# Kernel tuning notes

Hardware: AMD Instinct MI355X
Metric: run time of the kernel (lower is better)

## Reference

```python
import jax, jax.numpy as jnp
import numpy as np

T = 60          # fixed number of video frames (self.T)
EPS = 1e-5      # BatchNorm eps


def _lstm_cell(h, c, gates):
    # PyTorch gate order: input, forget, cell(g), output
    i, f, g, o = jnp.split(gates, 4, axis=-1)
    i = jax.nn.sigmoid(i)
    f = jax.nn.sigmoid(f)
    g = jnp.tanh(g)
    o = jax.nn.sigmoid(o)
    c = f * c + i * g
    h = o * jnp.tanh(c)
    return h, c


def setup_inputs() -> dict:
    key = jax.random.key(0)
    ks = jax.random.split(key, 12)
    B, H, Din, D = 256, 512, 2048, 512
    video_seq = jax.random.normal(ks[0], (B, T, Din), dtype=jnp.float32)
    captions = jax.random.randint(ks[1], (B, 20), 0, 10000, dtype=jnp.int32)
    s = 0.02
    return {
        'video_seq': video_seq,
        'captions': captions,
        'W_enc': jax.random.normal(ks[2], (D, Din), dtype=jnp.float32) * s,
        'b_enc': jnp.zeros((D,), jnp.float32),
        'gamma': jnp.ones((D,), jnp.float32),
        'beta': jnp.zeros((D,), jnp.float32),
        'w_attn': jax.random.normal(ks[3], (2 * H + T,), dtype=jnp.float32) * s,
        'b_attn': jnp.zeros((), jnp.float32),
        'W_ih': jax.random.normal(ks[4], (4 * H, D), dtype=jnp.float32) * s,
        'W_hh': jax.random.normal(ks[5], (4 * H, H), dtype=jnp.float32) * s,
        'b_ih': jnp.zeros((4 * H,), jnp.float32),
        'b_hh': jnp.zeros((4 * H,), jnp.float32),
    }


def reference(video_seq, captions, W_enc, b_enc, gamma, beta,
              w_attn, b_attn, W_ih, W_hh, b_ih, b_hh):
    H = W_hh.shape[1]
    B = video_seq.shape[0]
    caplen = captions.shape[1]

    # Dropout: eval mode (identity). Linear 2048 -> 512.
    v = jnp.einsum('btf,df->btd', video_seq, W_enc) + b_enc   # [B,T,512]
    # BatchNorm1d over channel dim (batch statistics, training-mode math)
    mean = v.mean(axis=(0, 1))
    var = v.var(axis=(0, 1))
    v = (v - mean) / jnp.sqrt(var + EPS) * gamma + beta       # [B,T,512]

    # Attention linear: concat([h,s,video_row]) @ w + b decomposes into
    # three independent dot products since h,s are broadcast over positions.
    w_h, w_s, w_v = w_attn[:H], w_attn[H:2 * H], w_attn[2 * H:]
    vscore = jnp.einsum('btd,t->bd', v, w_v) + b_attn         # [B,512]
    b_lstm = b_ih + b_hh

    v_t = jnp.moveaxis(v, 1, 0)                               # [T,B,512]

    def enc_step(carry, vt):
        h, c = carry
        scores = vscore + (h @ w_h + c @ w_s)[:, None]        # [B,512]
        alpha = jax.nn.softmax(scores, axis=1)
        x_t = alpha * vt                                      # [B,512]
        gates = x_t @ W_ih.T + h @ W_hh.T + b_lstm
        h, c = _lstm_cell(h, c, gates)
        return (h, c), h

    init = (jnp.zeros((B, H), v.dtype), jnp.zeros((B, H), v.dtype))
    (h, c), hs1 = jax.lax.scan(enc_step, init, v_t)           # hs1: [T,B,H]

    def pad_step(carry, _):
        h, c = carry
        gates = h @ W_hh.T + b_lstm                           # zero input
        h, c = _lstm_cell(h, c, gates)
        return (h, c), h

    _, hs2 = jax.lax.scan(pad_step, (h, c), None, length=caplen)
    hs = jnp.concatenate([hs1, hs2], axis=0)                  # [T+caplen,B,H]
    return jnp.transpose(hs, (1, 0, 2))                       # [B,T+caplen,H]
```

## Files before the change

### kernel.cpp

```cpp
#include <hip/hip_runtime.h>
#include <hip/hip_bf16.h>
#include <math.h>

#define B_    256
#define T_    60
#define TTOT  80
#define DIN   2048
#define D_    512
#define H_    512
#define G4    2048
#define M1    15360

typedef __bf16 bf16x8 __attribute__((ext_vector_type(8)));
typedef __bf16 bf16x4 __attribute__((ext_vector_type(4)));
typedef float  f32x4  __attribute__((ext_vector_type(4)));

__global__ void k_zero_u32(unsigned* __restrict__ p, int n) {
  int i = blockIdx.x * 256 + threadIdx.x;
  if (i < n) p[i] = 0u;
}

__global__ __launch_bounds__(256) void k_cvt(const float* __restrict__ s,
                                             __bf16* __restrict__ d, int n) {
  int i = (blockIdx.x * 256 + threadIdx.x) * 4;
  if (i >= n) return;
  float4 f = *(const float4*)(s + i);
  bf16x4 v;
  v[0] = (__bf16)f.x; v[1] = (__bf16)f.y; v[2] = (__bf16)f.z; v[3] = (__bf16)f.w;
  *(bf16x4*)(d + i) = v;
}

__global__ void k_bsum(const float* __restrict__ a, const float* __restrict__ b,
                       float* __restrict__ d) {
  int i = blockIdx.x * 256 + threadIdx.x;
  if (i < G4) d[i] = a[i] + b[i];
}

template<bool ALPHA, bool OUTBF, bool XT>
__global__ __launch_bounds__(256) void k_mm(const float* __restrict__ A, int lda,
                                            const __bf16* __restrict__ Bm,
                                            const float* __restrict__ bias0,
                                            const float* __restrict__ bias1,
                                            const float* __restrict__ alpha,
                                            void* __restrict__ Cout,
                                            int N, int K) {
  __shared__ __bf16 As[128 * 64];
  __shared__ __bf16 Bs[128 * 64];
  const int tid  = threadIdx.x;
  const int lane = tid & 63;
  const int wv   = tid >> 6;
  const int wm   = wv >> 1, wn = wv & 1;
  const int la   = lane & 15, lk = lane >> 4;

  int lin = blockIdx.y * gridDim.x + blockIdx.x;
  const int nwg = gridDim.x * gridDim.y;
  if ((nwg & 7) == 0) {
    int q = nwg >> 3;
    lin = (lin & 7) * q + (lin >> 3);
  }
  const int n0 = (lin % gridDim.x) * 128;
  const int m0 = (lin / gridDim.x) * 128;

  f32x4 acc[4][4];
  #pragma unroll
  for (int i = 0; i < 4; i++)
    #pragma unroll
    for (int j = 0; j < 4; j++) acc[i][j] = (f32x4){0.f, 0.f, 0.f, 0.f};

  for (int kt = 0; kt < K; kt += 64) {
    __syncthreads();
    #pragma unroll
    for (int i = 0; i < 4; i++) {
      int idx = tid + i * 256;
      int row = idx >> 3, gk = idx & 7;
      const float* src = A + (size_t)(m0 + row) * lda + kt + gk * 8;
      float4 f0 = *(const float4*)src;
      float4 f1 = *(const float4*)(src + 4);
      if (ALPHA) {
        int b = (m0 + row) / T_;
        const float* ap = alpha + (size_t)b * K + kt + gk * 8;
        float4 a0 = *(const float4*)ap;
        float4 a1 = *(const float4*)(ap + 4);
        f0.x *= a0.x; f0.y *= a0.y; f0.z *= a0.z; f0.w *= a0.w;
        f1.x *= a1.x; f1.y *= a1.y; f1.z *= a1.z; f1.w *= a1.w;
      }
      bf16x8 v;
      v[0] = (__bf16)f0.x; v[1] = (__bf16)f0.y; v[2] = (__bf16)f0.z; v[3] = (__bf16)f0.w;
      v[4] = (__bf16)f1.x; v[5] = (__bf16)f1.y; v[6] = (__bf16)f1.z; v[7] = (__bf16)f1.w;
      *(bf16x8*)(As + row * 64 + ((gk ^ (row & 7)) << 3)) = v;
    }
    #pragma unroll
    for (int i = 0; i < 4; i++) {
      int idx = tid + i * 256;
      int row = idx >> 3, gk = idx & 7;
      bf16x8 v = *(const bf16x8*)(Bm + (size_t)(n0 + row) * K + kt + gk * 8);
      *(bf16x8*)(Bs + row * 64 + ((gk ^ (row & 7)) << 3)) = v;
    }
    __syncthreads();
    #pragma unroll
    for (int ks = 0; ks < 2; ks++) {
      bf16x8 af[4], bfr[4];
      #pragma unroll
      for (int i = 0; i < 4; i++) {
        int row = wm * 64 + i * 16 + la;
        af[i] = *(const bf16x8*)(As + row * 64 + (((ks * 4 + lk) ^ (row & 7)) << 3));
      }
      #pragma unroll
      for (int j = 0; j < 4; j++) {
        int row = wn * 64 + j * 16 + la;
        bfr[j] = *(const bf16x8*)(Bs + row * 64 + (((ks * 4 + lk) ^ (row & 7)) << 3));
      }
      #pragma unroll
      for (int i = 0; i < 4; i++)
        #pragma unroll
        for (int j = 0; j < 4; j++)
          acc[i][j] = __builtin_amdgcn_mfma_f32_16x16x32_bf16(af[i], bfr[j], acc[i][j], 0, 0, 0);
    }
  }
  #pragma unroll
  for (int j = 0; j < 4; j++) {
    int col = n0 + wn * 64 + j * 16 + la;
    float bb = bias0[col] + (bias1 ? bias1[col] : 0.f);
    #pragma unroll
    for (int i = 0; i < 4; i++) {
      int rbase = m0 + wm * 64 + i * 16 + lk * 4;
      #pragma unroll
      for (int r = 0; r < 4; r++) {
        float v = acc[i][j][r] + bb;
        int m = rbase + r;
        if (XT) {
          int b = m / T_, tt = m % T_;
          int g = col >> 9, jj = col & 511;
          ((__bf16*)Cout)[(((size_t)tt * B_ + b) * 512 + jj) * 4 + g] = (__bf16)v;
        } else if (OUTBF) {
          ((__bf16*)Cout)[(size_t)m * N + col] = (__bf16)v;
        } else {
          ((float*)Cout)[(size_t)m * N + col] = v;
        }
      }
    }
  }
}

__global__ __launch_bounds__(256) void k_stats_partial(const float* __restrict__ V,
                                                       float* __restrict__ part) {
  const int blk = blockIdx.x;
  const int tid = threadIdx.x;
  float s0 = 0.f, s1 = 0.f, q0 = 0.f, q1 = 0.f;
  const float* p = V + (size_t)blk * 64 * D_;
  for (int r = 0; r < 64; r++) {
    float a = p[(size_t)r * D_ + tid];
    float b = p[(size_t)r * D_ + tid + 256];
    s0 += a; q0 += a * a;
    s1 += b; q1 += b * b;
  }
  part[(size_t)blk * 1024 + tid]             = s0;
  part[(size_t)blk * 1024 + tid + 256]       = s1;
  part[(size_t)blk * 1024 + 512 + tid]       = q0;
  part[(size_t)blk * 1024 + 512 + tid + 256] = q1;
}

__global__ __launch_bounds__(512) void k_stats_final(const float* __restrict__ part,
                                                     float* __restrict__ stats) {
  const int d = threadIdx.x;
  float s = 0.f, q = 0.f;
  for (int r = 0; r < 240; r++) {
    s += part[(size_t)r * 1024 + d];
    q += part[(size_t)r * 1024 + 512 + d];
  }
  float mean = s * (1.f / 15360.f);
  float var  = q * (1.f / 15360.f) - mean * mean;
  stats[d]        = mean;
  stats[512 + d]  = 1.f / sqrtf(var + 1e-5f);
}

__global__ __launch_bounds__(512) void k_norm_vscore(float* __restrict__ V,
                                                     const float* __restrict__ stats,
                                                     const float* __restrict__ gamma,
                                                     const float* __restrict__ beta,
                                                     const float* __restrict__ w_attn,
                                                     float* __restrict__ vscore) {
  const int b = blockIdx.x, d = threadIdx.x;
  __shared__ float wv[T_];
  if (d < T_) wv[d] = w_attn[2 * H_ + d];
  __syncthreads();
  const float mean = stats[d], rstd = stats[512 + d];
  const float ga = gamma[d], be = beta[d];
  float vs = 0.f;
  float* p = V + (size_t)b * T_ * D_ + d;
  for (int t = 0; t < T_; t++) {
    float x = p[(size_t)t * D_];
    float xn = (x - mean) * rstd * ga + be;
    p[(size_t)t * D_] = xn;
    vs += wv[t] * xn;
  }
  vscore[(size_t)b * D_ + d] = vs;
}

__global__ __launch_bounds__(512) void k_softmax(float* __restrict__ a) {
  const int b = blockIdx.x, d = threadIdx.x;
  __shared__ float red[8];
  float x = a[(size_t)b * D_ + d];
  float m = x;
  #pragma unroll
  for (int o = 32; o >= 1; o >>= 1) m = fmaxf(m, __shfl_xor(m, o));
  if ((d & 63) == 0) red[d >> 6] = m;
  __syncthreads();
  float M = red[0];
  #pragma unroll
  for (int w = 1; w < 8; w++) M = fmaxf(M, red[w]);
  float e = expf(x - M);
  float s = e;
  #pragma unroll
  for (int o = 32; o >= 1; o >>= 1) s += __shfl_xor(s, o);
  __syncthreads();
  if ((d & 63) == 0) red[d >> 6] = s;
  __syncthreads();
  float S = 0.f;
  #pragma unroll
  for (int w = 0; w < 8; w++) S += red[w];
  a[(size_t)b * D_ + d] = e / S;
}

__device__ __forceinline__ float sigf(float x) { return 1.f / (1.f + expf(-x)); }

__global__ __launch_bounds__(256) void k_rec(const __bf16* __restrict__ Whh,
                                             const __bf16* __restrict__ xW4,
                                             const float* __restrict__ bsum,
                                             __bf16* __restrict__ hbuf,
                                             float* __restrict__ out,
                                             unsigned* __restrict__ bar) {
  const int tid  = threadIdx.x;
  const int lane = tid & 63;
  const int widx = tid >> 6;
  const int grp  = blockIdx.x & 7;
  const int wg   = blockIdx.x >> 3;
  const int B0   = grp * 32;
  const int j0   = wg * 16;
  const int la   = lane & 15, lk = lane >> 4;

  __shared__ __bf16 wslab[4 * 16 * 520];
  __shared__ __bf16 hsin[16 * 520];
  __shared__ float  gatesL[4 * 256];

  #pragma unroll
  for (int it = 0; it < 16; it++) {
    bf16x8 v = *(const bf16x8*)(Whh + ((size_t)(widx * 512 + j0 + it)) * 512 + lane * 8);
    *(bf16x8*)(wslab + (widx * 16 + it) * 520 + lane * 8) = v;
  }

  const int cb = tid >> 4;
  const int cj = tid & 15;
  float bsl[4];
  #pragma unroll
  for (int g = 0; g < 4; g++) bsl[g] = bsum[g * 512 + j0 + cj];

  float creg[2] = {0.f, 0.f};
  unsigned* slots = bar + (size_t)grp * 64 * 32;

  bf16x4 xv[2];
  #pragma unroll
  for (int s = 0; s < 2; s++)
    xv[s] = *(const bf16x4*)(xW4 + (((size_t)(B0 + s * 16 + cb)) * 512 + j0 + cj) * 4);

  for (int t = 0; t < TTOT; t++) {
    const __bf16* hin  = hbuf + (size_t)(t & 1) * (B_ * H_);
    __bf16*       hout = hbuf + (size_t)((t + 1) & 1) * (B_ * H_);

    #pragma unroll
    for (int s = 0; s < 2; s++) {
      const int s16 = s * 16;

      if (t > 0) {
        if (tid < 32) {
          while (__hip_atomic_load(slots + (tid * 2 + s) * 32, __ATOMIC_RELAXED,
                                   __HIP_MEMORY_SCOPE_AGENT) < (unsigned)t)
            __builtin_amdgcn_s_sleep(1);
        }
        __syncthreads();

        unsigned long long vbuf[8];
        #pragma unroll
        for (int it = 0; it < 8; it++) {
          int idx = tid + it * 256;
          int row = idx >> 7, col4 = (idx & 127) * 4;
          vbuf[it] = __hip_atomic_load(
              (const unsigned long long*)(hin + (size_t)(B0 + s16 + row) * H_ + col4),
              __ATOMIC_RELAXED, __HIP_MEMORY_SCOPE_AGENT);
        }
        #pragma unroll
        for (int it = 0; it < 8; it++) {
          int idx = tid + it * 256;
          int row = idx >> 7, col4 = (idx & 127) * 4;
          *(unsigned long long*)(hsin + row * 520 + col4) = vbuf[it];
        }
        __syncthreads();

        f32x4 acc = (f32x4){0.f, 0.f, 0.f, 0.f};
        #pragma unroll
        for (int ks = 0; ks < 16; ks++) {
          bf16x8 w = *(const bf16x8*)(wslab + (widx * 16 + la) * 520 + ks * 32 + lk * 8);
          bf16x8 a = *(const bf16x8*)(hsin + la * 520 + ks * 32 + lk * 8);
          acc = __builtin_amdgcn_mfma_f32_16x16x32_bf16(a, w, acc, 0, 0, 0);
        }
        #pragma unroll
        for (int r = 0; r < 4; r++)
          gatesL[widx * 256 + (lk * 4 + r) * 16 + la] = acc[r];
        __syncthreads();
      }

      float p[4];
      #pragma unroll
      for (int g = 0; g < 4; g++)
        p[g] = (t > 0 ? gatesL[g * 256 + tid] : 0.f) + (float)xv[s][g];
      float gi = sigf(p[0]), gf = sigf(p[1]), gg = tanhf(p[2]), go = sigf(p[3]);
      float cn = gf * creg[s] + gi * gg;
      creg[s] = cn;
      float hn = go * tanhf(cn);

      __bf16 hb = (__bf16)hn;
      __hip_atomic_store((unsigned short*)(hout + (size_t)(B0 + s16 + cb) * H_ + j0 + cj),
                         *(unsigned short*)&hb,
                         __ATOMIC_RELAXED, __HIP_MEMORY_SCOPE_AGENT);
      asm volatile("s_waitcnt vmcnt(0)" ::: "memory");
      __syncthreads();
      if (tid == 0)
        __hip_atomic_store(slots + (wg * 2 + s) * 32, (unsigned)(t + 1),
                           __ATOMIC_RELAXED, __HIP_MEMORY_SCOPE_AGENT);

      out[((size_t)(B0 + s16 + cb) * TTOT + t) * D_ + j0 + cj] = hn;
      if (t + 1 < T_) {
        xv[s] = *(const bf16x4*)(xW4 + (((size_t)(t + 1) * B_ + B0 + s16 + cb) * 512 + j0 + cj) * 4);
      } else {
        #pragma unroll
        for (int g = 0; g < 4; g++) xv[s][g] = (__bf16)bsl[g];
      }
    }
  }
}

extern "C" void kernel_launch(void* const* d_in, const int* in_sizes, int n_in,
                              void* d_out, int out_size, void* d_ws, size_t ws_size,
                              hipStream_t stream) {
  const float* video  = (const float*)d_in[0];
  const float* W_enc  = (const float*)d_in[2];
  const float* b_enc  = (const float*)d_in[3];
  const float* gamma  = (const float*)d_in[4];
  const float* beta   = (const float*)d_in[5];
  const float* w_attn = (const float*)d_in[6];
  const float* W_ih   = (const float*)d_in[8];
  const float* W_hh   = (const float*)d_in[9];
  const float* b_ih   = (const float*)d_in[10];
  const float* b_hh   = (const float*)d_in[11];
  float* out = (float*)d_out;

  float*    base  = (float*)d_ws;
  float*    V     = base;                    size_t off = (size_t)M1 * D_;
  float*    part  = base + off;              off += 240 * 1024;
  float*    stats = base + off;              off += 1024;
  float*    alpha = base + off;              off += (size_t)B_ * D_;
  float*    bsum  = base + off;              off += G4;
  __bf16*   hbuf  = (__bf16*)(base + off);   off += (size_t)2 * B_ * H_ / 2;
  unsigned* bar   = (unsigned*)(base + off); off += 16384;
  __bf16*   xWbf  = (__bf16*)(base + off);   off += (size_t)M1 * G4 / 2;
  __bf16*   Wencb = (__bf16*)(base + off);   off += (size_t)D_ * DIN / 2;
  __bf16*   Wihb  = (__bf16*)(base + off);   off += (size_t)G4 * H_ / 2;
  __bf16*   Whhb  = (__bf16*)(base + off);   off += (size_t)G4 * H_ / 2;

  k_cvt<<<1024, 256, 0, stream>>>(W_enc, Wencb, D_ * DIN);
  k_cvt<<<1024, 256, 0, stream>>>(W_ih, Wihb, G4 * H_);
  k_cvt<<<1024, 256, 0, stream>>>(W_hh, Whhb, G4 * H_);
  k_bsum<<<8, 256, 0, stream>>>(b_ih, b_hh, bsum);

  k_zero_u32<<<64, 256, 0, stream>>>(bar, 16384);

  k_mm<false, false, false><<<dim3(4, 120), 256, 0, stream>>>(
      video, DIN, Wencb, b_enc, nullptr, nullptr, V, D_, DIN);

  k_stats_partial<<<240, 256, 0, stream>>>(V, part);
  k_stats_final<<<1, 512, 0, stream>>>(part, stats);
  k_norm_vscore<<<B_, 512, 0, stream>>>(V, stats, gamma, beta, w_attn, alpha);
  k_softmax<<<B_, 512, 0, stream>>>(alpha);

  k_mm<true, true, true><<<dim3(16, 120), 256, 0, stream>>>(
      V, D_, Wihb, b_ih, b_hh, alpha, (void*)xWbf, G4, D_);

  k_rec<<<256, 256, 0, stream>>>(Whhb, xWbf, bsum, hbuf, out, bar);
}
```

Baseline: 548.8 us.

## Collapse recurrent LSTM block to single wavefront with register-held h fragments

The persistent recurrent kernel now runs one 64-thread wavefront per block instead of four. That single wave computes all four gate tiles with MFMA, and it loads the h operand directly from global memory into registers rather than staging it through shared memory. This removes several block-wide barriers and an LDS round trip on the serial critical path, and output h is written as 8-byte chunks through a small staging tile. It also adds a bounded spin loop on the inter-block flags. The trade-off is four times more MFMA work per wave and per-lane global loads of h that are less well coalesced.

New measurement: 705.4 us. 1.29x slower.

```diff
diff --git a/kernel.cpp b/kernel.cpp
--- a/kernel.cpp
+++ b/kernel.cpp
@@ -224,44 +224,42 @@
 
 __device__ __forceinline__ float sigf(float x) { return 1.f / (1.f + expf(-x)); }
 
-__global__ __launch_bounds__(256) void k_rec(const __bf16* __restrict__ Whh,
-                                             const __bf16* __restrict__ xW4,
-                                             const float* __restrict__ bsum,
-                                             __bf16* __restrict__ hbuf,
-                                             float* __restrict__ out,
-                                             unsigned* __restrict__ bar) {
+__global__ __launch_bounds__(64) void k_rec(const __bf16* __restrict__ Whh,
+                                            const __bf16* __restrict__ xW4,
+                                            const float* __restrict__ bsum,
+                                            __bf16* __restrict__ hbuf,
+                                            float* __restrict__ out,
+                                            unsigned* __restrict__ bar) {
   const int tid  = threadIdx.x;
-  const int lane = tid & 63;
-  const int widx = tid >> 6;
   const int grp  = blockIdx.x & 7;
   const int wg   = blockIdx.x >> 3;
   const int B0   = grp * 32;
   const int j0   = wg * 16;
-  const int la   = lane & 15, lk = lane >> 4;
-
-  __shared__ __bf16 wslab[4 * 16 * 520];
-  __shared__ __bf16 hsin[16 * 520];
-  __shared__ float  gatesL[4 * 256];
-
-  #pragma unroll
-  for (int it = 0; it < 16; it++) {
-    bf16x8 v = *(const bf16x8*)(Whh + ((size_t)(widx * 512 + j0 + it)) * 512 + lane * 8);
-    *(bf16x8*)(wslab + (widx * 16 + it) * 520 + lane * 8) = v;
-  }
-
-  const int cb = tid >> 4;
-  const int cj = tid & 15;
+  const int la   = tid & 15, lk = tid >> 4;
+
+  __shared__ __bf16 wslab[4 * 16 * 528];
+  __shared__ __bf16 hstage[16][16];
+
+  for (int r = 0; r < 64; r++) {
+    int g = r >> 4, jr = r & 15;
+    bf16x8 v = *(const bf16x8*)(Whh + ((size_t)(g * 512 + j0 + jr)) * 512 + tid * 8);
+    *(bf16x8*)(wslab + r * 528 + tid * 8) = v;
+  }
+  __syncthreads();
+
   float bsl[4];
   #pragma unroll
-  for (int g = 0; g < 4; g++) bsl[g] = bsum[g * 512 + j0 + cj];
-
-  float creg[2] = {0.f, 0.f};
+  for (int g = 0; g < 4; g++) bsl[g] = bsum[g * 512 + j0 + la];
+
+  float creg[2][4] = {{0.f,0.f,0.f,0.f},{0.f,0.f,0.f,0.f}};
   unsigned* slots = bar + (size_t)grp * 64 * 32;
 
-  bf16x4 xv[2];
+  bf16x4 xv[2][4];
   #pragma unroll
   for (int s = 0; s < 2; s++)
-    xv[s] = *(const bf16x4*)(xW4 + (((size_t)(B0 + s * 16 + cb)) * 512 + j0 + cj) * 4);
+    #pragma unroll
+    for (int r = 0; r < 4; r++)
+      xv[s][r] = *(const bf16x4*)(xW4 + (((size_t)(B0 + s * 16 + lk * 4 + r)) * 512 + j0 + la) * 4);
 
   for (int t = 0; t < TTOT; t++) {
     const __bf16* hin  = hbuf + (size_t)(t & 1) * (B_ * H_);
@@ -271,70 +269,84 @@
     for (int s = 0; s < 2; s++) {
       const int s16 = s * 16;
 
+      f32x4 acc[4];
+      #pragma unroll
+      for (int g = 0; g < 4; g++) acc[g] = (f32x4){0.f, 0.f, 0.f, 0.f};
+
       if (t > 0) {
         if (tid < 32) {
-          while (__hip_atomic_load(slots + (tid * 2 + s) * 32, __ATOMIC_RELAXED,
-                                   __HIP_MEMORY_SCOPE_AGENT) < (unsigned)t)
+          for (int it = 0; it < (1 << 22); it++) {
+            if (__hip_atomic_load(slots + (tid * 2 + s) * 32, __ATOMIC_RELAXED,
+                                  __HIP_MEMORY_SCOPE_AGENT) >= (unsigned)t)
+              break;
             __builtin_amdgcn_s_sleep(1);
+          }
         }
-        __syncthreads();
-
-        unsigned long long vbuf[8];
-        #pragma unroll
-        for (int it = 0; it < 8; it++) {
-          int idx = tid + it * 256;
-          int row = idx >> 7, col4 = (idx & 127) * 4;
-          vbuf[it] = __hip_atomic_load(
-              (const unsigned long long*)(hin + (size_t)(B0 + s16 + row) * H_ + col4),
-              __ATOMIC_RELAXED, __HIP_MEMORY_SCOPE_AGENT);
-        }
-        #pragma unroll
-        for (int it = 0; it < 8; it++) {
-          int idx = tid + it * 256;
-          int row = idx >> 7, col4 = (idx & 127) * 4;
-          *(unsigned long long*)(hsin + row * 520 + col4) = vbuf[it];
-        }
-        __syncthreads();
-
-        f32x4 acc = (f32x4){0.f, 0.f, 0.f, 0.f};
+
+        union { unsigned long long u[2]; bf16x8 v; } afr[16];
+        const unsigned long long* hrow =
+            (const unsigned long long*)(hin + (size_t)(B0 + s16 + la) * H_);
         #pragma unroll
         for (int ks = 0; ks < 16; ks++) {
-          bf16x8 w = *(const bf16x8*)(wslab + (widx * 16 + la) * 520 + ks * 32 + lk * 8);
-          bf16x8 a = *(const bf16x8*)(hsin + la * 520 + ks * 32 + lk * 8);
-          acc = __builtin_amdgcn_mfma_f32_16x16x32_bf16(a, w, acc, 0, 0, 0);
+          afr[ks].u[0] = __hip_atomic_load(hrow + ks * 8 + lk * 2, __ATOMIC_RELAXED,
+                                           __HIP_MEMORY_SCOPE_AGENT);
+          afr[ks].u[1] = __hip_atomic_load(hrow + ks * 8 + lk * 2 + 1, __ATOMIC_RELAXED,
+                                           __HIP_MEMORY_SCOPE_AGENT);
         }
+
         #pragma unroll
-        for (int r = 0; r < 4; r++)
-          gatesL[widx * 256 + (lk * 4 + r) * 16 + la] = acc[r];
-        __syncthreads();
-      }
-
-      float p[4];
-      #pragma unroll
-      for (int g = 0; g < 4; g++)
-        p[g] = (t > 0 ? gatesL[g * 256 + tid] : 0.f) + (float)xv[s][g];
-      float gi = sigf(p[0]), gf = sigf(p[1]), gg = tanhf(p[2]), go = sigf(p[3]);
-      float cn = gf * creg[s] + gi * gg;
-      creg[s] = cn;
-      float hn = go * tanhf(cn);
-
-      __bf16 hb = (__bf16)hn;
-      __hip_atomic_store((unsigned short*)(hout + (size_t)(B0 + s16 + cb) * H_ + j0 + cj),
-                         *(unsigned short*)&hb,
-                         __ATOMIC_RELAXED, __HIP_MEMORY_SCOPE_AGENT);
+        for (int ks = 0; ks < 16; ks++) {
+          #pragma unroll
+          for (int g = 0; g < 4; g++) {
+            bf16x8 w = *(const bf16x8*)(wslab + (g * 16 + la) * 528 + ks * 32 + lk * 8);
+            acc[g] = __builtin_amdgcn_mfma_f32_16x16x32_bf16(afr[ks].v, w, acc[g], 0, 0, 0);
+          }
+        }
+      }
+
+      float hnv[4];
+      #pragma unroll
+      for (int r = 0; r < 4; r++) {
+        float gi = sigf(acc[0][r] + (float)xv[s][r][0]);
+        float gf = sigf(acc[1][r] + (float)xv[s][r][1]);
+        float gg = tanhf(acc[2][r] + (float)xv[s][r][2]);
+        float go = sigf(acc[3][r] + (float)xv[s][r][3]);
+        float cn = gf * creg[s][r] + gi * gg;
+        creg[s][r] = cn;
+        float hn = go * tanhf(cn);
+        hnv[r] = hn;
+        hstage[lk * 4 + r][la] = (__bf16)hn;
+      }
+      __syncthreads();
+
+      {
+        int row = tid >> 2, ch = tid & 3;
+        __hip_atomic_store(
+            (unsigned long long*)(hout + (size_t)(B0 + s16 + row) * H_ + j0 + ch * 4),
+            *(const unsigned long long*)&hstage[row][ch * 4],
+            __ATOMIC_RELAXED, __HIP_MEMORY_SCOPE_AGENT);
+      }
       asm volatile("s_waitcnt vmcnt(0)" ::: "memory");
-      __syncthreads();
       if (tid == 0)
         __hip_atomic_store(slots + (wg * 2 + s) * 32, (unsigned)(t + 1),
                            __ATOMIC_RELAXED, __HIP_MEMORY_SCOPE_AGENT);
 
-      out[((size_t)(B0 + s16 + cb) * TTOT + t) * D_ + j0 + cj] = hn;
+      #pragma unroll
+      for (int r = 0; r < 4; r++)
+        out[((size_t)(B0 + s16 + lk * 4 + r) * TTOT + t) * D_ + j0 + la] = hnv[r];
+
       if (t + 1 < T_) {
-        xv[s] = *(const bf16x4*)(xW4 + (((size_t)(t + 1) * B_ + B0 + s16 + cb) * 512 + j0 + cj) * 4);
+        #pragma unroll
+        for (int r = 0; r < 4; r++)
+          xv[s][r] = *(const bf16x4*)(xW4 +
+              (((size_t)(t + 1) * B_ + B0 + s16 + lk * 4 + r) * 512 + j0 + la) * 4);
       } else {
         #pragma unroll
-        for (int g = 0; g < 4; g++) xv[s][g] = (__bf16)bsl[g];
-      }
+        for (int r = 0; r < 4; r++)
+          #pragma unroll
+          for (int g = 0; g < 4; g++) xv[s][r][g] = (__bf16)bsl[g];
+      }
+      __syncthreads();
     }
   }
 }
@@ -385,5 +397,5 @@
   k_mm<true, true, true><<<dim3(16, 120), 256, 0, stream>>>(
       V, D_, Wihb, b_ih, b_hh, alpha, (void*)xWbf, G4, D_);
 
-  k_rec<<<256, 256, 0, stream>>>(Whhb, xWbf, bsum, hbuf, out, bar);
-}
+  k_rec<<<256, 64, 0, stream>>>(Whhb, xWbf, bsum, hbuf, out, bar);
+}
```

## Merge per-half recurrent sync into one step barrier and fuse prep kernels

Applied to the files above, without the earlier changes.

The recurrent kernel now waits once per timestep on both batch halves and computes both 16-row MFMA tiles together. It loads h directly from global into registers instead of staging it through shared memory, and publishes both halves' flags after a single barrier. This halves the number of cross-block synchronisations and LDS round-trips per step. The spin-wait now has a bounded iteration count. Separately, the weight conversions, bias sum and flag zeroing are fused into one launch, and softmax is fused into the normalisation kernel, cutting launch count.

Result: slower. 906.0 us (+65.1%).

```diff
diff --git a/kernel.cpp b/kernel.cpp
--- a/kernel.cpp
+++ b/kernel.cpp
@@ -15,25 +15,34 @@
 typedef __bf16 bf16x4 __attribute__((ext_vector_type(4)));
 typedef float  f32x4  __attribute__((ext_vector_type(4)));
 
-__global__ void k_zero_u32(unsigned* __restrict__ p, int n) {
-  int i = blockIdx.x * 256 + threadIdx.x;
-  if (i < n) p[i] = 0u;
-}
-
-__global__ __launch_bounds__(256) void k_cvt(const float* __restrict__ s,
-                                             __bf16* __restrict__ d, int n) {
-  int i = (blockIdx.x * 256 + threadIdx.x) * 4;
-  if (i >= n) return;
-  float4 f = *(const float4*)(s + i);
-  bf16x4 v;
-  v[0] = (__bf16)f.x; v[1] = (__bf16)f.y; v[2] = (__bf16)f.z; v[3] = (__bf16)f.w;
-  *(bf16x4*)(d + i) = v;
-}
-
-__global__ void k_bsum(const float* __restrict__ a, const float* __restrict__ b,
-                       float* __restrict__ d) {
-  int i = blockIdx.x * 256 + threadIdx.x;
-  if (i < G4) d[i] = a[i] + b[i];
+__global__ __launch_bounds__(256) void k_prep(const float* __restrict__ We,
+                                              const float* __restrict__ Wi,
+                                              const float* __restrict__ Wh,
+                                              __bf16* __restrict__ Web,
+                                              __bf16* __restrict__ Wib,
+                                              __bf16* __restrict__ Whb,
+                                              const float* __restrict__ bi,
+                                              const float* __restrict__ bh,
+                                              float* __restrict__ bsum,
+                                              unsigned* __restrict__ flags) {
+  const int blk = blockIdx.x, tid = threadIdx.x;
+  if (blk < 3072) {
+    const float* s; __bf16* d; int base;
+    if (blk < 1024)      { s = We; d = Web; base = blk; }
+    else if (blk < 2048) { s = Wi; d = Wib; base = blk - 1024; }
+    else                 { s = Wh; d = Whb; base = blk - 2048; }
+    int i = (base * 256 + tid) * 4;
+    float4 f = *(const float4*)(s + i);
+    bf16x4 v;
+    v[0] = (__bf16)f.x; v[1] = (__bf16)f.y; v[2] = (__bf16)f.z; v[3] = (__bf16)f.w;
+    *(bf16x4*)(d + i) = v;
+  } else if (blk < 3080) {
+    int i = (blk - 3072) * 256 + tid;
+    bsum[i] = bi[i] + bh[i];
+  } else {
+    int i = (blk - 3080) * 256 + tid;
+    flags[i] = 0u;
+  }
 }
 
 template<bool ALPHA, bool OUTBF, bool XT>
@@ -174,14 +183,15 @@
   stats[512 + d]  = 1.f / sqrtf(var + 1e-5f);
 }
 
-__global__ __launch_bounds__(512) void k_norm_vscore(float* __restrict__ V,
-                                                     const float* __restrict__ stats,
-                                                     const float* __restrict__ gamma,
-                                                     const float* __restrict__ beta,
-                                                     const float* __restrict__ w_attn,
-                                                     float* __restrict__ vscore) {
+__global__ __launch_bounds__(512) void k_norm_alpha(float* __restrict__ V,
+                                                    const float* __restrict__ stats,
+                                                    const float* __restrict__ gamma,
+                                                    const float* __restrict__ beta,
+                                                    const float* __restrict__ w_attn,
+                                                    float* __restrict__ alpha) {
   const int b = blockIdx.x, d = threadIdx.x;
   __shared__ float wv[T_];
+  __shared__ float red[8];
   if (d < T_) wv[d] = w_attn[2 * H_ + d];
   __syncthreads();
   const float mean = stats[d], rstd = stats[512 + d];
@@ -194,14 +204,7 @@
     p[(size_t)t * D_] = xn;
     vs += wv[t] * xn;
   }
-  vscore[(size_t)b * D_ + d] = vs;
-}
-
-__global__ __launch_bounds__(512) void k_softmax(float* __restrict__ a) {
-  const int b = blockIdx.x, d = threadIdx.x;
-  __shared__ float red[8];
-  float x = a[(size_t)b * D_ + d];
-  float m = x;
+  float m = vs;
   #pragma unroll
   for (int o = 32; o >= 1; o >>= 1) m = fmaxf(m, __shfl_xor(m, o));
   if ((d & 63) == 0) red[d >> 6] = m;
@@ -209,7 +212,7 @@
   float M = red[0];
   #pragma unroll
   for (int w = 1; w < 8; w++) M = fmaxf(M, red[w]);
-  float e = expf(x - M);
+  float e = expf(vs - M);
   float s = e;
   #pragma unroll
   for (int o = 32; o >= 1; o >>= 1) s += __shfl_xor(s, o);
@@ -219,17 +222,17 @@
   float S = 0.f;
   #pragma unroll
   for (int w = 0; w < 8; w++) S += red[w];
-  a[(size_t)b * D_ + d] = e / S;
+  alpha[(size_t)b * D_ + d] = e / S;
 }
 
 __device__ __forceinline__ float sigf(float x) { return 1.f / (1.f + expf(-x)); }
 
-__global__ __launch_bounds__(256) void k_rec(const __bf16* __restrict__ Whh,
-                                             const __bf16* __restrict__ xW4,
-                                             const float* __restrict__ bsum,
-                                             __bf16* __restrict__ hbuf,
-                                             float* __restrict__ out,
-                                             unsigned* __restrict__ bar) {
+__global__ __launch_bounds__(256, 1) void k_rec(const __bf16* __restrict__ Whh,
+                                                const __bf16* __restrict__ xW4,
+                                                const float* __restrict__ bsum,
+                                                __bf16* __restrict__ hbuf,
+                                                float* __restrict__ out,
+                                                unsigned* __restrict__ bar) {
   const int tid  = threadIdx.x;
   const int lane = tid & 63;
   const int widx = tid >> 6;
@@ -240,8 +243,7 @@
   const int la   = lane & 15, lk = lane >> 4;
 
   __shared__ __bf16 wslab[4 * 16 * 520];
-  __shared__ __bf16 hsin[16 * 520];
-  __shared__ float  gatesL[4 * 256];
+  __shared__ float  gatesL[2][1024];
 
   #pragma unroll
   for (int it = 0; it < 16; it++) {
@@ -263,78 +265,100 @@
   for (int s = 0; s < 2; s++)
     xv[s] = *(const bf16x4*)(xW4 + (((size_t)(B0 + s * 16 + cb)) * 512 + j0 + cj) * 4);
 
+  __syncthreads();
+
   for (int t = 0; t < TTOT; t++) {
     const __bf16* hin  = hbuf + (size_t)(t & 1) * (B_ * H_);
     __bf16*       hout = hbuf + (size_t)((t + 1) & 1) * (B_ * H_);
 
+    if (t > 0) {
+      if (tid < 64) {
+        unsigned* p = slots + ((tid & 31) * 2 + (tid >> 5)) * 32;
+        for (int it = 0; it < (1 << 22); it++) {
+          if (__hip_atomic_load(p, __ATOMIC_RELAXED,
+                                __HIP_MEMORY_SCOPE_AGENT) >= (unsigned)t)
+            break;
+          __builtin_amdgcn_s_sleep(1);
+        }
+      }
+      __syncthreads();
+
+      const unsigned long long* r0 =
+          (const unsigned long long*)(hin + (size_t)(B0 + la) * H_);
+      const unsigned long long* r1 =
+          (const unsigned long long*)(hin + (size_t)(B0 + 16 + la) * H_);
+      unsigned long long a0[32], a1[32];
+      #pragma unroll
+      for (int ks = 0; ks < 16; ks++) {
+        a0[2 * ks]     = __hip_atomic_load(r0 + ks * 8 + lk * 2, __ATOMIC_RELAXED,
+                                           __HIP_MEMORY_SCOPE_AGENT);
+        a0[2 * ks + 1] = __hip_atomic_load(r0 + ks * 8 + lk * 2 + 1, __ATOMIC_RELAXED,
+                                           __HIP_MEMORY_SCOPE_AGENT);
+      }
+      #pragma unroll
+      for (int ks = 0; ks < 16; ks++) {
+        a1[2 * ks]     = __hip_atomic_load(r1 + ks * 8 + lk * 2, __ATOMIC_RELAXED,
+                                           __HIP_MEMORY_SCOPE_AGENT);
+        a1[2 * ks + 1] = __hip_atomic_load(r1 + ks * 8 + lk * 2 + 1, __ATOMIC_RELAXED,
+                                           __HIP_MEMORY_SCOPE_AGENT);
+      }
+
+      f32x4 acc0 = (f32x4){0.f, 0.f, 0.f, 0.f};
+      f32x4 acc1 = (f32x4){0.f, 0.f, 0.f, 0.f};
+      #pragma unroll
+      for (int ks = 0; ks < 16; ks++) {
+        bf16x8 w = *(const bf16x8*)(wslab + (widx * 16 + la) * 520 + ks * 32 + lk * 8);
+        union { unsigned long long u[2]; bf16x8 v; } f0, f1;
+        f0.u[0] = a0[2 * ks]; f0.u[1] = a0[2 * ks + 1];
+        f1.u[0] = a1[2 * ks]; f1.u[1] = a1[2 * ks + 1];
+        acc0 = __builtin_amdgcn_mfma_f32_16x16x32_bf16(f0.v, w, acc0, 0, 0, 0);
+        acc1 = __builtin_amdgcn_mfma_f32_16x16x32_bf16(f1.v, w, acc1, 0, 0, 0);
+      }
+      #pragma unroll
+      for (int r = 0; r < 4; r++) {
+        gatesL[0][widx * 256 + (lk * 4 + r) * 16 + la] = acc0[r];
+        gatesL[1][widx * 256 + (lk * 4 + r) * 16 + la] = acc1[r];
+      }
+      __syncthreads();
+    }
+
+    float hn_[2];
     #pragma unroll
     for (int s = 0; s < 2; s++) {
-      const int s16 = s * 16;
-
-      if (t > 0) {
-        if (tid < 32) {
-          while (__hip_atomic_load(slots + (tid * 2 + s) * 32, __ATOMIC_RELAXED,
-                                   __HIP_MEMORY_SCOPE_AGENT) < (unsigned)t)
-            __builtin_amdgcn_s_sleep(1);
-        }
-        __syncthreads();
-
-        unsigned long long vbuf[8];
-        #pragma unroll
-        for (int it = 0; it < 8; it++) {
-          int idx = tid + it * 256;
-          int row = idx >> 7, col4 = (idx & 127) * 4;
-          vbuf[it] = __hip_atomic_load(
-              (const unsigned long long*)(hin + (size_t)(B0 + s16 + row) * H_ + col4),
-              __ATOMIC_RELAXED, __HIP_MEMORY_SCOPE_AGENT);
-        }
-        #pragma unroll
-        for (int it = 0; it < 8; it++) {
-          int idx = tid + it * 256;
-          int row = idx >> 7, col4 = (idx & 127) * 4;
-          *(unsigned long long*)(hsin + row * 520 + col4) = vbuf[it];
-        }
-        __syncthreads();
-
-        f32x4 acc = (f32x4){0.f, 0.f, 0.f, 0.f};
-        #pragma unroll
-        for (int ks = 0; ks < 16; ks++) {
-          bf16x8 w = *(const bf16x8*)(wslab + (widx * 16 + la) * 520 + ks * 32 + lk * 8);
-          bf16x8 a = *(const bf16x8*)(hsin + la * 520 + ks * 32 + lk * 8);
-          acc = __builtin_amdgcn_mfma_f32_16x16x32_bf16(a, w, acc, 0, 0, 0);
-        }
-        #pragma unroll
-        for (int r = 0; r < 4; r++)
-          gatesL[widx * 256 + (lk * 4 + r) * 16 + la] = acc[r];
-        __syncthreads();
-      }
-
       float p[4];
       #pragma unroll
       for (int g = 0; g < 4; g++)
-        p[g] = (t > 0 ? gatesL[g * 256 + tid] : 0.f) + (float)xv[s][g];
+        p[g] = (t > 0 ? gatesL[s][g * 256 + tid] : 0.f) + (float)xv[s][g];
       float gi = sigf(p[0]), gf = sigf(p[1]), gg = tanhf(p[2]), go = sigf(p[3]);
       float cn = gf * creg[s] + gi * gg;
       creg[s] = cn;
       float hn = go * tanhf(cn);
-
+      hn_[s] = hn;
       __bf16 hb = (__bf16)hn;
-      __hip_atomic_store((unsigned short*)(hout + (size_t)(B0 + s16 + cb) * H_ + j0 + cj),
-                         *(unsigned short*)&hb,
+      __hip_atomic_store(
+          (unsigned short*)(hout + (size_t)(B0 + s * 16 + cb) * H_ + j0 + cj),
+          *(unsigned short*)&hb, __ATOMIC_RELAXED, __HIP_MEMORY_SCOPE_AGENT);
+    }
+    asm volatile("s_waitcnt vmcnt(0)" ::: "memory");
+    __syncthreads();
+    if (tid < 2)
+      __hip_atomic_store(slots + (wg * 2 + tid) * 32, (unsigned)(t + 1),
                          __ATOMIC_RELAXED, __HIP_MEMORY_SCOPE_AGENT);
-      asm volatile("s_waitcnt vmcnt(0)" ::: "memory");
-      __syncthreads();
-      if (tid == 0)
-        __hip_atomic_store(slots + (wg * 2 + s) * 32, (unsigned)(t + 1),
-                           __ATOMIC_RELAXED, __HIP_MEMORY_SCOPE_AGENT);
-
-      out[((size_t)(B0 + s16 + cb) * TTOT + t) * D_ + j0 + cj] = hn;
-      if (t + 1 < T_) {
-        xv[s] = *(const bf16x4*)(xW4 + (((size_t)(t + 1) * B_ + B0 + s16 + cb) * 512 + j0 + cj) * 4);
-      } else {
+
+    #pragma unroll
+    for (int s = 0; s < 2; s++)
+      out[((size_t)(B0 + s * 16 + cb) * TTOT + t) * D_ + j0 + cj] = hn_[s];
+
+    if (t + 1 < T_) {
+      #pragma unroll
+      for (int s = 0; s < 2; s++)
+        xv[s] = *(const bf16x4*)(xW4 +
+            (((size_t)(t + 1) * B_ + B0 + s * 16 + cb) * 512 + j0 + cj) * 4);
+    } else {
+      #pragma unroll
+      for (int s = 0; s < 2; s++)
         #pragma unroll
         for (int g = 0; g < 4; g++) xv[s][g] = (__bf16)bsl[g];
-      }
     }
   }
 }
@@ -367,20 +391,15 @@
   __bf16*   Wihb  = (__bf16*)(base + off);   off += (size_t)G4 * H_ / 2;
   __bf16*   Whhb  = (__bf16*)(base + off);   off += (size_t)G4 * H_ / 2;
 
-  k_cvt<<<1024, 256, 0, stream>>>(W_enc, Wencb, D_ * DIN);
-  k_cvt<<<1024, 256, 0, stream>>>(W_ih, Wihb, G4 * H_);
-  k_cvt<<<1024, 256, 0, stream>>>(W_hh, Whhb, G4 * H_);
-  k_bsum<<<8, 256, 0, stream>>>(b_ih, b_hh, bsum);
-
-  k_zero_u32<<<64, 256, 0, stream>>>(bar, 16384);
+  k_prep<<<3144, 256, 0, stream>>>(W_enc, W_ih, W_hh, Wencb, Wihb, Whhb,
+                                   b_ih, b_hh, bsum, bar);
 
   k_mm<false, false, false><<<dim3(4, 120), 256, 0, stream>>>(
       video, DIN, Wencb, b_enc, nullptr, nullptr, V, D_, DIN);
 
   k_stats_partial<<<240, 256, 0, stream>>>(V, part);
   k_stats_final<<<1, 512, 0, stream>>>(part, stats);
-  k_norm_vscore<<<B_, 512, 0, stream>>>(V, stats, gamma, beta, w_attn, alpha);
-  k_softmax<<<B_, 512, 0, stream>>>(alpha);
+  k_norm_alpha<<<B_, 512, 0, stream>>>(V, stats, gamma, beta, w_attn, alpha);
 
   k_mm<true, true, true><<<dim3(16, 120), 256, 0, stream>>>(
       V, D_, Wihb, b_ih, b_hh, alpha, (void*)xWbf, G4, D_);
```
